# Performance work log

Measured on AMD Instinct MI355X. Metric: run time of the kernel, lower is better.

Reference implementation:

```python
import jax, jax.numpy as jnp
import numpy as np

B, S, H = 64, 512, 768   # n_blocks, seq_len, hidden
C, M = 50, 2000          # n_characters, n_mentions
T = B * S                # total_seq_len
NEG_INF = -jnp.inf


def setup_inputs() -> dict:
    key = jax.random.key(0)
    ks = jax.random.split(key, 16)
    story_embeddings = jax.random.normal(ks[0], (B, S, H), dtype=jnp.float32)

    # additive log masks: 0.0 = allowed token, -inf = blocked (matches softmax(score + mask))
    names_bin = jax.random.bernoulli(ks[1], 0.05, (C, S)).at[:, 0].set(True)  # every char has >=1 name token
    names_mask = jnp.where(names_bin, 0.0, NEG_INF).astype(jnp.float32)

    utt_bin = jax.random.bernoulli(ks[2], 0.02, (C, T))
    utt_bin = utt_bin.at[40:].set(False)  # chars 40..49 have no utterances -> nan_to_num path
    utterances_mask = jnp.where(utt_bin, 0.0, NEG_INF).astype(jnp.float32)

    men_bin = jax.random.bernoulli(ks[3], 0.01, (M, T)).at[:, 0].set(True)
    mentions_mask = jnp.where(men_bin, 0.0, NEG_INF).astype(jnp.float32)

    mention_character_ids = jax.random.randint(ks[4], (M,), 0, 45, dtype=jnp.int32)  # chars 45..49 mention-less

    def lin(k):
        return 0.02 * jax.random.normal(k, (H,), dtype=jnp.float32)

    return {
        "story_embeddings": story_embeddings,
        "names_mask": names_mask,
        "utterances_mask": utterances_mask,
        "mentions_mask": mentions_mask,
        "mention_character_ids": mention_character_ids,
        "w_name_tok": lin(ks[5]), "b_name_tok": jnp.float32(0.0),
        "w_name": lin(ks[6]), "b_name": jnp.float32(0.0),
        "w_men_tok": lin(ks[7]), "b_men_tok": jnp.float32(0.0),
        "w_men": lin(ks[8]), "b_men": jnp.float32(0.0),
        "w_utt": lin(ks[9]), "b_utt": jnp.float32(0.0),
        "w_comb": lin(ks[10]), "b_comb": jnp.float32(0.0),
    }


def reference(story_embeddings, names_mask, utterances_mask, mentions_mask,
              mention_character_ids, w_name_tok, b_name_tok, w_name, b_name,
              w_men_tok, b_men_tok, w_men, b_men, w_utt, b_utt, w_comb, b_comb):
    n_char = names_mask.shape[0]
    n_blocks, seqlen, hidden = story_embeddings.shape
    se_flat = story_embeddings.reshape(n_blocks * seqlen, hidden)  # [T,H]

    # ---- name representation ----
    nts = story_embeddings @ w_name_tok + b_name_tok                       # [B,S]
    n_attn = jax.nn.softmax(nts[None, :, :] + names_mask[:, None, :], axis=2)  # [C,B,S]
    names_emb = jnp.einsum('cbs,bsh->cbh', n_attn, story_embeddings)       # [C,B,H]
    n_score = names_emb @ w_name + b_name                                  # [C,B]
    name_e = jnp.einsum('cb,cbh->ch', jax.nn.softmax(n_score, axis=1), names_emb)

    # ---- mention representation (segment softmax over mentions per character) ----
    mts = se_flat @ w_men_tok + b_men_tok                                  # [T]
    m_attn = jax.nn.softmax(mentions_mask + mts[None, :], axis=1)          # [M,T]
    m_emb = m_attn @ se_flat                                               # [M,H]
    m_score = m_emb @ w_men + b_men                                        # [M]
    seg = mention_character_ids
    seg_max = jax.ops.segment_max(m_score, seg, num_segments=n_char)       # [C]
    ex = jnp.exp(m_score - seg_max[seg])                                   # [M]
    den = jax.ops.segment_sum(ex, seg, num_segments=n_char)                # [C]
    mw = ex / den[seg]                                                     # [M]
    mention_e = jax.ops.segment_sum(mw[:, None] * m_emb, seg, num_segments=n_char)  # [C,H]; empty chars -> 0

    # ---- utterance representation ----
    uts = se_flat @ w_utt + b_utt                                          # [T]
    u_attn = jnp.nan_to_num(jax.nn.softmax(utterances_mask + uts[None, :], axis=1), nan=0.0)
    utt_e = u_attn @ se_flat                                               # [C,H]

    # ---- combine ----
    emb = jnp.stack([name_e, mention_e, utt_e], axis=1)                    # [C,3,H]
    score = emb @ w_comb + b_comb                                          # [C,3]
    has_mention = jax.ops.segment_sum(jnp.ones_like(m_score), seg, num_segments=n_char) > 0
    has_utt = jnp.any(utterances_mask == 0, axis=1)
    zeros = jnp.zeros((n_char,), dtype=score.dtype)
    mask = jnp.stack([zeros,
                      jnp.where(has_mention, 0.0, NEG_INF := -jnp.inf),
                      jnp.where(has_utt, 0.0, -jnp.inf)], axis=1)          # [C,3]
    attn = jax.nn.softmax(score + mask, axis=1)
    return jnp.einsum('ck,ckh->ch', attn, emb)                             # [C,H]
```

## Files before the change

kernel.cpp:

```cpp
#include <hip/hip_runtime.h>
#include <cmath>

#define Bn 64
#define Sn 512
#define Hn 768
#define Cn 50
#define Mn 2000
#define Tn (Bn*Sn)
#define MCAP 1024
#define NP 128
#define TC 256
#define HT 128

__global__ __launch_bounds__(256) void k_proj(
    const float* __restrict__ se,
    const float* __restrict__ w_ntok, const float* __restrict__ b_ntok,
    const float* __restrict__ w_name,
    const float* __restrict__ w_mtok, const float* __restrict__ b_mtok,
    const float* __restrict__ w_men,
    const float* __restrict__ w_utt, const float* __restrict__ b_utt,
    const float* __restrict__ w_comb,
    float* __restrict__ nts, float* __restrict__ p_name,
    float* __restrict__ mts, float* __restrict__ p_men,
    float* __restrict__ uts, float* __restrict__ p_comb)
{
    int wave = threadIdx.x >> 6, lane = threadIdx.x & 63;
    int r = blockIdx.x * 4 + wave;
    const float4* se4 = (const float4*)(se + (size_t)r * Hn);
    const float4* w0 = (const float4*)w_ntok;
    const float4* w1 = (const float4*)w_name;
    const float4* w2 = (const float4*)w_mtok;
    const float4* w3 = (const float4*)w_men;
    const float4* w4 = (const float4*)w_utt;
    const float4* w5 = (const float4*)w_comb;
    float s0=0,s1=0,s2=0,s3=0,s4=0,s5=0;
#pragma unroll
    for (int k = 0; k < 3; k++) {
        int i = lane + 64*k;
        float4 v = se4[i];
        float4 a;
        a = w0[i]; s0 += v.x*a.x + v.y*a.y + v.z*a.z + v.w*a.w;
        a = w1[i]; s1 += v.x*a.x + v.y*a.y + v.z*a.z + v.w*a.w;
        a = w2[i]; s2 += v.x*a.x + v.y*a.y + v.z*a.z + v.w*a.w;
        a = w3[i]; s3 += v.x*a.x + v.y*a.y + v.z*a.z + v.w*a.w;
        a = w4[i]; s4 += v.x*a.x + v.y*a.y + v.z*a.z + v.w*a.w;
        a = w5[i]; s5 += v.x*a.x + v.y*a.y + v.z*a.z + v.w*a.w;
    }
#pragma unroll
    for (int off = 32; off >= 1; off >>= 1) {
        s0 += __shfl_xor(s0, off); s1 += __shfl_xor(s1, off);
        s2 += __shfl_xor(s2, off); s3 += __shfl_xor(s3, off);
        s4 += __shfl_xor(s4, off); s5 += __shfl_xor(s5, off);
    }
    if (lane == 0) {
        nts[r]    = s0 + b_ntok[0];
        p_name[r] = s1;
        mts[r]    = s2 + b_mtok[0];
        p_men[r]  = s3;
        uts[r]    = s4 + b_utt[0];
        p_comb[r] = s5;
    }
}

__global__ __launch_bounds__(256) void k_nu(
    const float* __restrict__ nm_mask, const float* __restrict__ umask,
    const float* __restrict__ nts, const float* __restrict__ uts,
    const float* __restrict__ p_name, const float* __restrict__ p_comb,
    const float* __restrict__ b_name_p,
    float* __restrict__ bw, float* __restrict__ m1n, float* __restrict__ denn,
    float* __restrict__ sc0,
    float* __restrict__ m1u, float* __restrict__ denu, float* __restrict__ sc2)
{
    int tid = threadIdx.x;
    int wv = tid >> 6, lane = tid & 63;
    if (blockIdx.x < Cn) {
        int c = blockIdx.x;
        __shared__ float sScore[Bn], sScn[Bn];
        float nmv[8];
#pragma unroll
        for (int k = 0; k < 8; k++) nmv[k] = nm_mask[c*Sn + lane + 64*k];
        float bnp = b_name_p[0];
        for (int it = 0; it < 16; ++it) {
            int b = it*4 + wv;
            const float* nrow = nts    + b*Sn;
            const float* prow = p_name + b*Sn;
            const float* crow = p_comb + b*Sn;
            float v[8]; float mx = -INFINITY;
#pragma unroll
            for (int k = 0; k < 8; k++) {
                float val = nmv[k] + nrow[lane + 64*k];
                v[k] = val; mx = fmaxf(mx, val);
            }
#pragma unroll
            for (int off = 32; off >= 1; off >>= 1) mx = fmaxf(mx, __shfl_xor(mx, off));
            float d = 0, sn = 0, sc = 0;
#pragma unroll
            for (int k = 0; k < 8; k++) {
                float e = __expf(v[k] - mx);
                d += e; sn += e * prow[lane + 64*k]; sc += e * crow[lane + 64*k];
            }
#pragma unroll
            for (int off = 32; off >= 1; off >>= 1) {
                d += __shfl_xor(d, off); sn += __shfl_xor(sn, off); sc += __shfl_xor(sc, off);
            }
            if (lane == 0) {
                sScore[b] = sn/d + bnp;
                sScn[b]   = sc/d;
                m1n[c*Bn + b] = mx;
                denn[c*Bn + b] = d;
            }
        }
        __syncthreads();
        if (wv == 0) {
            float s = sScore[lane];
            float mx = s;
#pragma unroll
            for (int off = 32; off >= 1; off >>= 1) mx = fmaxf(mx, __shfl_xor(mx, off));
            float e = __expf(s - mx);
            float d = e, ss = e * sScn[lane];
#pragma unroll
            for (int off = 32; off >= 1; off >>= 1) { d += __shfl_xor(d, off); ss += __shfl_xor(ss, off); }
            bw[c*Bn + lane] = e/d;
            if (lane == 0) sc0[c] = ss/d;
        }
    } else {
        int c = blockIdx.x - Cn;
        __shared__ int scnt;
        __shared__ int   sT[MCAP];
        __shared__ float sV[MCAP];
        __shared__ float sr1[4], sr2[4], sr3[4];
        if (tid == 0) scnt = 0;
        __syncthreads();
        const float4* urow4 = (const float4*)(umask + (size_t)c * Tn);
        const float4* uts4  = (const float4*)uts;
        for (int k = 0; k < Tn/4/256; k++) {
            int i = tid + k*256;
            float4 f = urow4[i];
            float4 v = uts4[i];
            float fm[4] = {f.x, f.y, f.z, f.w};
            float vv[4] = {v.x, v.y, v.z, v.w};
#pragma unroll
            for (int j = 0; j < 4; j++) {
                if (fm[j] == 0.0f) {
                    int s = atomicAdd(&scnt, 1);
                    if (s < MCAP) { sT[s] = i*4 + j; sV[s] = vv[j]; }
                }
            }
        }
        __syncthreads();
        int n = (scnt < MCAP) ? scnt : MCAP;
        float mx = -INFINITY;
        for (int i = tid; i < n; i += 256) mx = fmaxf(mx, sV[i]);
#pragma unroll
        for (int off = 32; off >= 1; off >>= 1) mx = fmaxf(mx, __shfl_xor(mx, off));
        if (lane == 0) sr1[wv] = mx;
        __syncthreads();
        mx = fmaxf(fmaxf(sr1[0], sr1[1]), fmaxf(sr1[2], sr1[3]));
        float d = 0, nc = 0;
        for (int i = tid; i < n; i += 256) {
            float e = __expf(sV[i] - mx);
            d += e; nc += e * p_comb[sT[i]];
        }
#pragma unroll
        for (int off = 32; off >= 1; off >>= 1) { d += __shfl_xor(d, off); nc += __shfl_xor(nc, off); }
        if (lane == 0) { sr2[wv] = d; sr3[wv] = nc; }
        __syncthreads();
        if (tid == 0) {
            float dd = sr2[0]+sr2[1]+sr2[2]+sr2[3];
            float nn = sr3[0]+sr3[1]+sr3[2]+sr3[3];
            m1u[c]  = mx;
            denu[c] = dd;
            sc2[c]  = (dd > 0.f) ? nn/dd : 0.f;
        }
    }
}

__global__ __launch_bounds__(256) void k_mentions(
    const float* __restrict__ mmask, const float* __restrict__ mts,
    const float* __restrict__ p_men, const float* __restrict__ p_comb,
    const float* __restrict__ b_men_p,
    float* __restrict__ m_score, float* __restrict__ mcv,
    float* __restrict__ denm,
    int* __restrict__ midx, float* __restrict__ mwgt, int* __restrict__ mcnt)
{
    int m = blockIdx.x, tid = threadIdx.x;
    int wv = tid >> 6, lane = tid & 63;
    __shared__ int scnt;
    __shared__ int   sT[MCAP];
    __shared__ float sV[MCAP];
    __shared__ float sr1[4], sr2[4], sr3[4], sr4[4];
    if (tid == 0) scnt = 0;
    __syncthreads();
    const float4* row4 = (const float4*)(mmask + (size_t)m * Tn);
    const float4* mts4 = (const float4*)mts;
    for (int k = 0; k < Tn/4/256; k++) {
        int i = tid + k*256;
        float4 f = row4[i];
        float4 v = mts4[i];
        float fm[4] = {f.x, f.y, f.z, f.w};
        float vv[4] = {v.x, v.y, v.z, v.w};
#pragma unroll
        for (int j = 0; j < 4; j++) {
            if (fm[j] == 0.0f) {
                int s = atomicAdd(&scnt, 1);
                if (s < MCAP) { sT[s] = i*4 + j; sV[s] = vv[j]; }
            }
        }
    }
    __syncthreads();
    int n = (scnt < MCAP) ? scnt : MCAP;
    float mx = -INFINITY;
    for (int i = tid; i < n; i += 256) mx = fmaxf(mx, sV[i]);
#pragma unroll
    for (int off = 32; off >= 1; off >>= 1) mx = fmaxf(mx, __shfl_xor(mx, off));
    if (lane == 0) sr1[wv] = mx;
    __syncthreads();
    mx = fmaxf(fmaxf(sr1[0], sr1[1]), fmaxf(sr1[2], sr1[3]));
    float d = 0, nm = 0, nc = 0;
    int* gi = midx + (size_t)m * MCAP;
    float* gwp = mwgt + (size_t)m * MCAP;
    for (int i = tid; i < n; i += 256) {
        float e = __expf(sV[i] - mx);
        int t = sT[i];
        d += e; nm += e * p_men[t]; nc += e * p_comb[t];
        gi[i] = t; gwp[i] = e;
    }
#pragma unroll
    for (int off = 32; off >= 1; off >>= 1) {
        d += __shfl_xor(d, off); nm += __shfl_xor(nm, off); nc += __shfl_xor(nc, off);
    }
    if (lane == 0) { sr2[wv] = d; sr3[wv] = nm; sr4[wv] = nc; }
    __syncthreads();
    if (tid == 0) {
        float dd = sr2[0]+sr2[1]+sr2[2]+sr2[3];
        float sm = sr3[0]+sr3[1]+sr3[2]+sr3[3];
        float sc = sr4[0]+sr4[1]+sr4[2]+sr4[3];
        m_score[m] = sm/dd + b_men_p[0];
        mcv[m]     = sc/dd;
        denm[m]    = dd;
        mcnt[m]    = n;
    }
}

__global__ __launch_bounds__(256) void k_seg(
    const int* __restrict__ seg, const float* __restrict__ m_score, const float* __restrict__ mcv,
    float* __restrict__ segmax, float* __restrict__ segden, float* __restrict__ sc1)
{
    int c = blockIdx.x, tid = threadIdx.x;
    float mx = -INFINITY;
    for (int m = tid; m < Mn; m += 256)
        if (seg[m] == c) mx = fmaxf(mx, m_score[m]);
    __shared__ float sm[256];
    sm[tid] = mx; __syncthreads();
    for (int s = 128; s > 0; s >>= 1) { if (tid < s) sm[tid] = fmaxf(sm[tid], sm[tid+s]); __syncthreads(); }
    mx = sm[0];
    float d = 0, s1 = 0;
    if (mx != -INFINITY) {
        for (int m = tid; m < Mn; m += 256)
            if (seg[m] == c) { float e = __expf(m_score[m] - mx); d += e; s1 += e * mcv[m]; }
    }
    __shared__ float sd[256], ss[256];
    sd[tid] = d; ss[tid] = s1; __syncthreads();
    for (int s = 128; s > 0; s >>= 1) { if (tid < s) { sd[tid] += sd[tid+s]; ss[tid] += ss[tid+s]; } __syncthreads(); }
    if (tid == 0) {
        segmax[c] = mx;
        segden[c] = sd[0];
        sc1[c]    = (sd[0] > 0.f) ? ss[0]/sd[0] : 0.f;
    }
}

__device__ inline void combine_attn(float sc0v, float sc1v, float sc2v,
                                    float sdn, float dnu, float bc,
                                    float& a0, float& a1, float& a2)
{
    float s0 = sc0v + bc;
    bool hasm = sdn > 0.f, hasu = dnu > 0.f;
    float s1 = hasm ? sc1v + bc : -INFINITY;
    float s2 = hasu ? sc2v + bc : -INFINITY;
    float mx = fmaxf(s0, fmaxf(s1, s2));
    float e0 = __expf(s0 - mx);
    float e1 = hasm ? __expf(s1 - mx) : 0.f;
    float e2 = hasu ? __expf(s2 - mx) : 0.f;
    float dd = e0 + e1 + e2;
    a0 = e0/dd; a1 = e1/dd; a2 = e2/dd;
}

__global__ __launch_bounds__(256) void k_buildW(
    const float* __restrict__ nm_mask, const float* __restrict__ nts,
    const float* __restrict__ m1n, const float* __restrict__ denn,
    const float* __restrict__ bw,
    const float* __restrict__ umask, const float* __restrict__ uts,
    const float* __restrict__ m1u, const float* __restrict__ denu,
    const float* __restrict__ sc0, const float* __restrict__ sc1, const float* __restrict__ sc2,
    const float* __restrict__ segden, const float* __restrict__ b_comb_p,
    float* __restrict__ W)
{
    int c = blockIdx.y;
    float a0, a1, a2;
    combine_attn(sc0[c], sc1[c], sc2[c], segden[c], denu[c], b_comb_p[0], a0, a1, a2);
    int t0 = (blockIdx.x * 256 + threadIdx.x) * 4;
    int b = t0 >> 9;
    float4 um = *(const float4*)(umask + (size_t)c * Tn + t0);
    float cn = a0 * bw[c*Bn + b] / denn[c*Bn + b];
    float m1nc = m1n[c*Bn + b];
    float du = denu[c];
    float cu = (du > 0.f) ? a2 / du : 0.f;
    float m1uc = m1u[c];
    float umj[4] = {um.x, um.y, um.z, um.w};
    float rj[4];
#pragma unroll
    for (int j = 0; j < 4; j++) {
        int t = t0 + j;
        int s = t & (Sn-1);
        float w = 0.f;
        if (nm_mask[c*Sn + s] == 0.f) w += cn * __expf(nts[t] - m1nc);
        if (umj[j] == 0.f)            w += cu * __expf(uts[t] - m1uc);
        rj[j] = w;
    }
    *(float4*)(W + (size_t)c * Tn + t0) = make_float4(rj[0], rj[1], rj[2], rj[3]);
}

__global__ __launch_bounds__(64) void k_scatter_men(
    const int* __restrict__ midx, const float* __restrict__ mwgt, const int* __restrict__ mcnt,
    const int* __restrict__ seg,
    const float* __restrict__ m_score, const float* __restrict__ denm,
    const float* __restrict__ segmax, const float* __restrict__ segden,
    const float* __restrict__ sc0, const float* __restrict__ sc1, const float* __restrict__ sc2,
    const float* __restrict__ denu, const float* __restrict__ b_comb_p,
    float* __restrict__ W)
{
    int m = blockIdx.x, tid = threadIdx.x;
    int c = seg[m];
    float a0, a1, a2;
    combine_attn(sc0[c], sc1[c], sc2[c], segden[c], denu[c], b_comb_p[0], a0, a1, a2);
    float coef = a1 * __expf(m_score[m] - segmax[c]) / segden[c] / denm[m];
    int n = mcnt[m];
    const int* gi = midx + (size_t)m * MCAP;
    const float* gwp = mwgt + (size_t)m * MCAP;
    float* Wc = W + (size_t)c * Tn;
    for (int i = tid; i < n; i += 64)
        atomicAdd(&Wc[gi[i]], coef * gwp[i]);
}

__global__ __launch_bounds__(256) void k_out1(
    const float* __restrict__ W, const float* __restrict__ se, float* __restrict__ partial)
{
    int p = blockIdx.x;
    int h0 = blockIdx.y * HT;
    int tid = threadIdx.x;
    int x = tid & 31, y = tid >> 5;
    __shared__ float sW[56][64];
    __shared__ float sS[64][128];
    float4 acc[7];
#pragma unroll
    for (int i = 0; i < 7; i++) acc[i] = make_float4(0,0,0,0);
    for (int sub = 0; sub < 4; sub++) {
        int tbase = p*TC + sub*64;
        for (int i = tid; i < 896; i += 256) {
            int c = i >> 4, f = i & 15;
            float4 v = (c < Cn) ? *(const float4*)(W + (size_t)c * Tn + tbase + f*4)
                                : make_float4(0,0,0,0);
            *(float4*)&sW[c][f*4] = v;
        }
#pragma unroll
        for (int q = 0; q < 8; q++) {
            int idx = tid + q*256;
            int row = idx >> 5, col = idx & 31;
            *(float4*)&sS[row][col*4] =
                *(const float4*)(se + (size_t)(tbase + row) * Hn + h0 + col*4);
        }
        __syncthreads();
        for (int t = 0; t < 64; t++) {
            float4 v = *(const float4*)&sS[t][x*4];
#pragma unroll
            for (int cc = 0; cc < 7; cc++) {
                float w = sW[y*7 + cc][t];
                acc[cc].x += w*v.x; acc[cc].y += w*v.y;
                acc[cc].z += w*v.z; acc[cc].w += w*v.w;
            }
        }
        __syncthreads();
    }
#pragma unroll
    for (int cc = 0; cc < 7; cc++) {
        int c = y*7 + cc;
        if (c < Cn)
            *(float4*)(partial + ((size_t)p * Cn + c) * Hn + h0 + x*4) = acc[cc];
    }
}

__global__ __launch_bounds__(256) void k_out2(
    const float* __restrict__ partial, float* __restrict__ out)
{
    int cell = blockIdx.x * 256 + threadIdx.x;
    if (cell < Cn*Hn) {
        float s = 0.f;
#pragma unroll 8
        for (int p = 0; p < NP; p++)
            s += partial[(size_t)p * (Cn*Hn) + cell];
        out[cell] = s;
    }
}

extern "C" void kernel_launch(void* const* d_in, const int* in_sizes, int n_in,
                              void* d_out, int out_size, void* d_ws, size_t ws_size,
                              hipStream_t stream) {
    const float* se      = (const float*)d_in[0];
    const float* nm_mask = (const float*)d_in[1];
    const float* umask   = (const float*)d_in[2];
    const float* mmask   = (const float*)d_in[3];
    const int*   seg     = (const int*)  d_in[4];
    const float* w_ntok  = (const float*)d_in[5];
    const float* b_ntok  = (const float*)d_in[6];
    const float* w_name  = (const float*)d_in[7];
    const float* b_name  = (const float*)d_in[8];
    const float* w_mtok  = (const float*)d_in[9];
    const float* b_mtok  = (const float*)d_in[10];
    const float* w_men   = (const float*)d_in[11];
    const float* b_men   = (const float*)d_in[12];
    const float* w_utt   = (const float*)d_in[13];
    const float* b_utt   = (const float*)d_in[14];
    const float* w_comb  = (const float*)d_in[15];
    const float* b_comb  = (const float*)d_in[16];
    float* out = (float*)d_out;

    float* ws = (float*)d_ws;
    float* partial = ws;
    float* W       = partial + (size_t)NP*Cn*Hn;
    float* nts     = W + (size_t)Cn*Tn;
    float* p_name  = nts + Tn;
    float* mts     = p_name + Tn;
    float* p_men   = mts + Tn;
    float* uts     = p_men + Tn;
    float* p_comb  = uts + Tn;
    float* bw      = p_comb + Tn;
    float* m1n     = bw + Cn*Bn;
    float* denn    = m1n + Cn*Bn;
    float* m_score = denn + Cn*Bn;
    float* mcv     = m_score + Mn;
    float* denm    = mcv + Mn;
    float* mwgt    = denm + Mn;
    int*   midx    = (int*)(mwgt + (size_t)Mn*MCAP);
    int*   mcnt    = midx + (size_t)Mn*MCAP;
    float* segmax  = (float*)(mcnt + Mn);
    float* segden  = segmax + Cn;
    float* sc0     = segden + Cn;
    float* sc1     = sc0 + Cn;
    float* sc2     = sc1 + Cn;
    float* m1u     = sc2 + Cn;
    float* denu    = m1u + Cn;

    k_proj<<<Tn/4, 256, 0, stream>>>(se, w_ntok, b_ntok, w_name, w_mtok, b_mtok,
                                     w_men, w_utt, b_utt, w_comb,
                                     nts, p_name, mts, p_men, uts, p_comb);

    k_nu<<<2*Cn, 256, 0, stream>>>(nm_mask, umask, nts, uts, p_name, p_comb, b_name,
                                   bw, m1n, denn, sc0, m1u, denu, sc2);

    k_mentions<<<Mn, 256, 0, stream>>>(mmask, mts, p_men, p_comb, b_men,
                                       m_score, mcv, denm, midx, mwgt, mcnt);

    k_seg<<<Cn, 256, 0, stream>>>(seg, m_score, mcv, segmax, segden, sc1);

    k_buildW<<<dim3(Tn/1024, Cn), 256, 0, stream>>>(nm_mask, nts, m1n, denn, bw,
                                                    umask, uts, m1u, denu,
                                                    sc0, sc1, sc2, segden, b_comb, W);

    k_scatter_men<<<Mn, 64, 0, stream>>>(midx, mwgt, mcnt, seg, m_score, denm,
                                         segmax, segden, sc0, sc1, sc2, denu, b_comb, W);

    k_out1<<<dim3(NP, Hn/HT), 256, 0, stream>>>(W, se, partial);
    k_out2<<<(Cn*Hn + 255)/256, 256, 0, stream>>>(partial, out);
}
```

Before: 198.5 us.

## Split name softmax across blocks, merge utterance scan into mention scan, ballot compaction

Name-token softmax now runs as one wave per (character, block) pair over many blocks, where before 50 blocks each looped over all 64 story blocks. The utterance row scan is folded into the mention scan kernel, giving one launch of 2050 rows. The block-level name softmax is merged with the segment reduction into a small kernel. Per-element shared atomics in the compaction are replaced by wave ballot and popcount with one atomic per wave. The aim is more parallelism and less serial and atomic overhead, at the cost of an extra workspace buffer.

```diff
diff --git a/kernel.cpp b/kernel.cpp
--- a/kernel.cpp
+++ b/kernel.cpp
@@ -62,153 +62,95 @@
     }
 }
 
-__global__ __launch_bounds__(256) void k_nu(
-    const float* __restrict__ nm_mask, const float* __restrict__ umask,
-    const float* __restrict__ nts, const float* __restrict__ uts,
+__global__ __launch_bounds__(256) void k_names(
+    const float* __restrict__ nm_mask, const float* __restrict__ nts,
     const float* __restrict__ p_name, const float* __restrict__ p_comb,
     const float* __restrict__ b_name_p,
-    float* __restrict__ bw, float* __restrict__ m1n, float* __restrict__ denn,
-    float* __restrict__ sc0,
-    float* __restrict__ m1u, float* __restrict__ denu, float* __restrict__ sc2)
-{
-    int tid = threadIdx.x;
-    int wv = tid >> 6, lane = tid & 63;
-    if (blockIdx.x < Cn) {
-        int c = blockIdx.x;
-        __shared__ float sScore[Bn], sScn[Bn];
-        float nmv[8];
-#pragma unroll
-        for (int k = 0; k < 8; k++) nmv[k] = nm_mask[c*Sn + lane + 64*k];
-        float bnp = b_name_p[0];
-        for (int it = 0; it < 16; ++it) {
-            int b = it*4 + wv;
-            const float* nrow = nts    + b*Sn;
-            const float* prow = p_name + b*Sn;
-            const float* crow = p_comb + b*Sn;
-            float v[8]; float mx = -INFINITY;
-#pragma unroll
-            for (int k = 0; k < 8; k++) {
-                float val = nmv[k] + nrow[lane + 64*k];
-                v[k] = val; mx = fmaxf(mx, val);
-            }
-#pragma unroll
-            for (int off = 32; off >= 1; off >>= 1) mx = fmaxf(mx, __shfl_xor(mx, off));
-            float d = 0, sn = 0, sc = 0;
-#pragma unroll
-            for (int k = 0; k < 8; k++) {
-                float e = __expf(v[k] - mx);
-                d += e; sn += e * prow[lane + 64*k]; sc += e * crow[lane + 64*k];
-            }
-#pragma unroll
-            for (int off = 32; off >= 1; off >>= 1) {
-                d += __shfl_xor(d, off); sn += __shfl_xor(sn, off); sc += __shfl_xor(sc, off);
-            }
-            if (lane == 0) {
-                sScore[b] = sn/d + bnp;
-                sScn[b]   = sc/d;
-                m1n[c*Bn + b] = mx;
-                denn[c*Bn + b] = d;
-            }
-        }
-        __syncthreads();
-        if (wv == 0) {
-            float s = sScore[lane];
-            float mx = s;
-#pragma unroll
-            for (int off = 32; off >= 1; off >>= 1) mx = fmaxf(mx, __shfl_xor(mx, off));
-            float e = __expf(s - mx);
-            float d = e, ss = e * sScn[lane];
-#pragma unroll
-            for (int off = 32; off >= 1; off >>= 1) { d += __shfl_xor(d, off); ss += __shfl_xor(ss, off); }
-            bw[c*Bn + lane] = e/d;
-            if (lane == 0) sc0[c] = ss/d;
-        }
-    } else {
-        int c = blockIdx.x - Cn;
-        __shared__ int scnt;
-        __shared__ int   sT[MCAP];
-        __shared__ float sV[MCAP];
-        __shared__ float sr1[4], sr2[4], sr3[4];
-        if (tid == 0) scnt = 0;
-        __syncthreads();
-        const float4* urow4 = (const float4*)(umask + (size_t)c * Tn);
-        const float4* uts4  = (const float4*)uts;
-        for (int k = 0; k < Tn/4/256; k++) {
-            int i = tid + k*256;
-            float4 f = urow4[i];
-            float4 v = uts4[i];
-            float fm[4] = {f.x, f.y, f.z, f.w};
-            float vv[4] = {v.x, v.y, v.z, v.w};
-#pragma unroll
-            for (int j = 0; j < 4; j++) {
-                if (fm[j] == 0.0f) {
-                    int s = atomicAdd(&scnt, 1);
-                    if (s < MCAP) { sT[s] = i*4 + j; sV[s] = vv[j]; }
-                }
-            }
-        }
-        __syncthreads();
-        int n = (scnt < MCAP) ? scnt : MCAP;
-        float mx = -INFINITY;
-        for (int i = tid; i < n; i += 256) mx = fmaxf(mx, sV[i]);
-#pragma unroll
-        for (int off = 32; off >= 1; off >>= 1) mx = fmaxf(mx, __shfl_xor(mx, off));
-        if (lane == 0) sr1[wv] = mx;
-        __syncthreads();
-        mx = fmaxf(fmaxf(sr1[0], sr1[1]), fmaxf(sr1[2], sr1[3]));
-        float d = 0, nc = 0;
-        for (int i = tid; i < n; i += 256) {
-            float e = __expf(sV[i] - mx);
-            d += e; nc += e * p_comb[sT[i]];
-        }
-#pragma unroll
-        for (int off = 32; off >= 1; off >>= 1) { d += __shfl_xor(d, off); nc += __shfl_xor(nc, off); }
-        if (lane == 0) { sr2[wv] = d; sr3[wv] = nc; }
-        __syncthreads();
-        if (tid == 0) {
-            float dd = sr2[0]+sr2[1]+sr2[2]+sr2[3];
-            float nn = sr3[0]+sr3[1]+sr3[2]+sr3[3];
-            m1u[c]  = mx;
-            denu[c] = dd;
-            sc2[c]  = (dd > 0.f) ? nn/dd : 0.f;
-        }
-    }
-}
-
-__global__ __launch_bounds__(256) void k_mentions(
+    float* __restrict__ n_score, float* __restrict__ sc_n,
+    float* __restrict__ m1n, float* __restrict__ denn)
+{
+    int wave = threadIdx.x >> 6, lane = threadIdx.x & 63;
+    int idx = blockIdx.x * 4 + wave;
+    int c = idx >> 6, b = idx & 63;
+    float v[8];
+    float mx = -INFINITY;
+#pragma unroll
+    for (int k = 0; k < 8; k++) {
+        int s = lane + 64*k;
+        float val = nm_mask[c*Sn + s] + nts[b*Sn + s];
+        v[k] = val;
+        mx = fmaxf(mx, val);
+    }
+#pragma unroll
+    for (int off = 32; off >= 1; off >>= 1) mx = fmaxf(mx, __shfl_xor(mx, off));
+    float d = 0, sn = 0, sc = 0;
+#pragma unroll
+    for (int k = 0; k < 8; k++) {
+        int s = lane + 64*k;
+        int t = b*Sn + s;
+        float e = __expf(v[k] - mx);
+        d += e; sn += e * p_name[t]; sc += e * p_comb[t];
+    }
+#pragma unroll
+    for (int off = 32; off >= 1; off >>= 1) {
+        d += __shfl_xor(d, off); sn += __shfl_xor(sn, off); sc += __shfl_xor(sc, off);
+    }
+    if (lane == 0) {
+        n_score[idx] = sn / d + b_name_p[0];
+        sc_n[idx]    = sc / d;
+        m1n[idx]     = mx;
+        denn[idx]    = d;
+    }
+}
+
+__global__ __launch_bounds__(256) void k_scan(
     const float* __restrict__ mmask, const float* __restrict__ mts,
     const float* __restrict__ p_men, const float* __restrict__ p_comb,
     const float* __restrict__ b_men_p,
-    float* __restrict__ m_score, float* __restrict__ mcv,
-    float* __restrict__ denm,
-    int* __restrict__ midx, float* __restrict__ mwgt, int* __restrict__ mcnt)
-{
-    int m = blockIdx.x, tid = threadIdx.x;
+    const float* __restrict__ umask, const float* __restrict__ uts,
+    float* __restrict__ m_score, float* __restrict__ mcv, float* __restrict__ denm,
+    int* __restrict__ midx, float* __restrict__ mwgt, int* __restrict__ mcnt,
+    float* __restrict__ m1u, float* __restrict__ denu, float* __restrict__ sc2)
+{
+    int tid = threadIdx.x;
     int wv = tid >> 6, lane = tid & 63;
+    bool isU = blockIdx.x >= Mn;
+    int row = isU ? (blockIdx.x - Mn) : blockIdx.x;
+
     __shared__ int scnt;
     __shared__ int   sT[MCAP];
     __shared__ float sV[MCAP];
     __shared__ float sr1[4], sr2[4], sr3[4], sr4[4];
     if (tid == 0) scnt = 0;
     __syncthreads();
-    const float4* row4 = (const float4*)(mmask + (size_t)m * Tn);
-    const float4* mts4 = (const float4*)mts;
+
+    const float4* row4  = (const float4*)((isU ? umask : mmask) + (size_t)row * Tn);
+    const float4* vals4 = (const float4*)(isU ? uts : mts);
+
     for (int k = 0; k < Tn/4/256; k++) {
         int i = tid + k*256;
         float4 f = row4[i];
-        float4 v = mts4[i];
+        float4 v = vals4[i];
         float fm[4] = {f.x, f.y, f.z, f.w};
         float vv[4] = {v.x, v.y, v.z, v.w};
 #pragma unroll
         for (int j = 0; j < 4; j++) {
-            if (fm[j] == 0.0f) {
-                int s = atomicAdd(&scnt, 1);
-                if (s < MCAP) { sT[s] = i*4 + j; sV[s] = vv[j]; }
+            bool act = (fm[j] == 0.0f);
+            unsigned long long bm = __ballot(act);
+            if (bm) {
+                int tot = __popcll(bm);
+                int pos = __popcll(bm & ((1ull << lane) - 1ull));
+                int base;
+                if (lane == 0) base = atomicAdd(&scnt, tot);
+                base = __shfl(base, 0);
+                int s = base + pos;
+                if (act && s < MCAP) { sT[s] = i*4 + j; sV[s] = vv[j]; }
             }
         }
     }
     __syncthreads();
     int n = (scnt < MCAP) ? scnt : MCAP;
+
     float mx = -INFINITY;
     for (int i = tid; i < n; i += 256) mx = fmaxf(mx, sV[i]);
 #pragma unroll
@@ -216,14 +158,22 @@
     if (lane == 0) sr1[wv] = mx;
     __syncthreads();
     mx = fmaxf(fmaxf(sr1[0], sr1[1]), fmaxf(sr1[2], sr1[3]));
+
     float d = 0, nm = 0, nc = 0;
-    int* gi = midx + (size_t)m * MCAP;
-    float* gwp = mwgt + (size_t)m * MCAP;
-    for (int i = tid; i < n; i += 256) {
-        float e = __expf(sV[i] - mx);
-        int t = sT[i];
-        d += e; nm += e * p_men[t]; nc += e * p_comb[t];
-        gi[i] = t; gwp[i] = e;
+    if (!isU) {
+        int* gi = midx + (size_t)row * MCAP;
+        float* gwp = mwgt + (size_t)row * MCAP;
+        for (int i = tid; i < n; i += 256) {
+            float e = __expf(sV[i] - mx);
+            int t = sT[i];
+            d += e; nm += e * p_men[t]; nc += e * p_comb[t];
+            gi[i] = t; gwp[i] = e;
+        }
+    } else {
+        for (int i = tid; i < n; i += 256) {
+            float e = __expf(sV[i] - mx);
+            d += e; nc += e * p_comb[sT[i]];
+        }
     }
 #pragma unroll
     for (int off = 32; off >= 1; off >>= 1) {
@@ -235,37 +185,64 @@
         float dd = sr2[0]+sr2[1]+sr2[2]+sr2[3];
         float sm = sr3[0]+sr3[1]+sr3[2]+sr3[3];
         float sc = sr4[0]+sr4[1]+sr4[2]+sr4[3];
-        m_score[m] = sm/dd + b_men_p[0];
-        mcv[m]     = sc/dd;
-        denm[m]    = dd;
-        mcnt[m]    = n;
-    }
-}
-
-__global__ __launch_bounds__(256) void k_seg(
+        if (!isU) {
+            m_score[row] = sm/dd + b_men_p[0];
+            mcv[row]     = sc/dd;
+            denm[row]    = dd;
+            mcnt[row]    = n;
+        } else {
+            m1u[row]  = mx;
+            denu[row] = dd;
+            sc2[row]  = (dd > 0.f) ? sc/dd : 0.f;
+        }
+    }
+}
+
+__global__ __launch_bounds__(256) void k_small(
+    const float* __restrict__ n_score, const float* __restrict__ sc_n,
     const int* __restrict__ seg, const float* __restrict__ m_score, const float* __restrict__ mcv,
+    float* __restrict__ bw, float* __restrict__ sc0,
     float* __restrict__ segmax, float* __restrict__ segden, float* __restrict__ sc1)
 {
-    int c = blockIdx.x, tid = threadIdx.x;
-    float mx = -INFINITY;
-    for (int m = tid; m < Mn; m += 256)
-        if (seg[m] == c) mx = fmaxf(mx, m_score[m]);
-    __shared__ float sm[256];
-    sm[tid] = mx; __syncthreads();
-    for (int s = 128; s > 0; s >>= 1) { if (tid < s) sm[tid] = fmaxf(sm[tid], sm[tid+s]); __syncthreads(); }
-    mx = sm[0];
-    float d = 0, s1 = 0;
-    if (mx != -INFINITY) {
+    int tid = threadIdx.x;
+    if (blockIdx.x < Cn) {
+        int c = blockIdx.x;
+        if (tid < 64) {
+            int lane = tid;
+            int idx = c*Bn + lane;
+            float v = n_score[idx];
+            float mx = v;
+#pragma unroll
+            for (int off = 32; off >= 1; off >>= 1) mx = fmaxf(mx, __shfl_xor(mx, off));
+            float e = __expf(v - mx);
+            float d = e, s = e * sc_n[idx];
+#pragma unroll
+            for (int off = 32; off >= 1; off >>= 1) { d += __shfl_xor(d, off); s += __shfl_xor(s, off); }
+            bw[idx] = e / d;
+            if (lane == 0) sc0[c] = s / d;
+        }
+    } else {
+        int c = blockIdx.x - Cn;
+        float mx = -INFINITY;
         for (int m = tid; m < Mn; m += 256)
-            if (seg[m] == c) { float e = __expf(m_score[m] - mx); d += e; s1 += e * mcv[m]; }
-    }
-    __shared__ float sd[256], ss[256];
-    sd[tid] = d; ss[tid] = s1; __syncthreads();
-    for (int s = 128; s > 0; s >>= 1) { if (tid < s) { sd[tid] += sd[tid+s]; ss[tid] += ss[tid+s]; } __syncthreads(); }
-    if (tid == 0) {
-        segmax[c] = mx;
-        segden[c] = sd[0];
-        sc1[c]    = (sd[0] > 0.f) ? ss[0]/sd[0] : 0.f;
+            if (seg[m] == c) mx = fmaxf(mx, m_score[m]);
+        __shared__ float sm[256];
+        sm[tid] = mx; __syncthreads();
+        for (int s = 128; s > 0; s >>= 1) { if (tid < s) sm[tid] = fmaxf(sm[tid], sm[tid+s]); __syncthreads(); }
+        mx = sm[0];
+        float d = 0, s1 = 0;
+        if (mx != -INFINITY) {
+            for (int m = tid; m < Mn; m += 256)
+                if (seg[m] == c) { float e = __expf(m_score[m] - mx); d += e; s1 += e * mcv[m]; }
+        }
+        __shared__ float sd[256], ss[256];
+        sd[tid] = d; ss[tid] = s1; __syncthreads();
+        for (int s = 128; s > 0; s >>= 1) { if (tid < s) { sd[tid] += sd[tid+s]; ss[tid] += ss[tid+s]; } __syncthreads(); }
+        if (tid == 0) {
+            segmax[c] = mx;
+            segden[c] = sd[0];
+            sc1[c]    = (sd[0] > 0.f) ? ss[0]/sd[0] : 0.f;
+        }
     }
 }
 
@@ -433,7 +410,9 @@
     float* p_men   = mts + Tn;
     float* uts     = p_men + Tn;
     float* p_comb  = uts + Tn;
-    float* bw      = p_comb + Tn;
+    float* n_score = p_comb + Tn;
+    float* sc_n    = n_score + Cn*Bn;
+    float* bw      = sc_n + Cn*Bn;
     float* m1n     = bw + Cn*Bn;
     float* denn    = m1n + Cn*Bn;
     float* m_score = denn + Cn*Bn;
@@ -454,13 +433,16 @@
                                      w_men, w_utt, b_utt, w_comb,
                                      nts, p_name, mts, p_men, uts, p_comb);
 
-    k_nu<<<2*Cn, 256, 0, stream>>>(nm_mask, umask, nts, uts, p_name, p_comb, b_name,
-                                   bw, m1n, denn, sc0, m1u, denu, sc2);
-
-    k_mentions<<<Mn, 256, 0, stream>>>(mmask, mts, p_men, p_comb, b_men,
-                                       m_score, mcv, denm, midx, mwgt, mcnt);
-
-    k_seg<<<Cn, 256, 0, stream>>>(seg, m_score, mcv, segmax, segden, sc1);
+    k_names<<<(Cn*Bn)/4, 256, 0, stream>>>(nm_mask, nts, p_name, p_comb, b_name,
+                                           n_score, sc_n, m1n, denn);
+
+    k_scan<<<Mn + Cn, 256, 0, stream>>>(mmask, mts, p_men, p_comb, b_men,
+                                        umask, uts,
+                                        m_score, mcv, denm, midx, mwgt, mcnt,
+                                        m1u, denu, sc2);
+
+    k_small<<<2*Cn, 256, 0, stream>>>(n_score, sc_n, seg, m_score, mcv,
+                                      bw, sc0, segmax, segden, sc1);
 
     k_buildW<<<dim3(Tn/1024, Cn), 256, 0, stream>>>(nm_mask, nts, m1n, denn, bw,
                                                     umask, uts, m1u, denu,
```

New measurement: 195.0 us. Within noise of the previous version (-1.8%).
